# Kernel tuning notes

Hardware: AMD Instinct MI355X
Metric: run time of the kernel (lower is better)

## Reference

```python
import jax, jax.numpy as jnp
import numpy as np

N = 100_000          # nodes
E = 3_200_000        # edges
DIM = 64             # filt_conv_dimension
L = 3                # filt_conv_number
MAX_DEG = 64         # embedding table size = MAX_DEG + 1
SUM_DIMS = DIM * (L + 1)  # 256, fc input
BN_EPS = 1e-5
NEG_SLOPE = 0.01


def _leaky(x):
    return jnp.where(x >= 0, x, NEG_SLOPE * x)


def _batchnorm(x, g, b):
    # training-mode BN over the node axis
    mu = jnp.mean(x, axis=0, keepdims=True)
    var = jnp.var(x, axis=0, keepdims=True)
    return g * (x - mu) * jax.lax.rsqrt(var + BN_EPS) + b


def setup_inputs() -> dict:
    key = jax.random.key(0)
    ks = jax.random.split(key, 16)
    s = 0.05
    inp = {
        "node_deg": jax.random.randint(ks[0], (N,), 0, MAX_DEG, dtype=jnp.int32),
        "edge_index": jax.random.randint(ks[1], (2, E), 0, N, dtype=jnp.int32),
        "embed_deg": jax.random.normal(ks[2], (MAX_DEG + 1, DIM), jnp.float32) * s,
        "eps": jnp.zeros((L,), jnp.float32),
        "W1": jax.random.normal(ks[3], (L, DIM, DIM), jnp.float32) * s,
        "b1": jnp.zeros((L, DIM), jnp.float32),
        "W2": jax.random.normal(ks[4], (L, DIM, DIM), jnp.float32) * s,
        "b2": jnp.zeros((L, DIM), jnp.float32),
        "bn_g": jnp.ones((L, DIM), jnp.float32),
        "bn_b": jnp.zeros((L, DIM), jnp.float32),
        "fc_W1": jax.random.normal(ks[5], (SUM_DIMS, DIM), jnp.float32) * s,
        "fc_b1": jnp.zeros((DIM,), jnp.float32),
        "fc_bn_g": jnp.ones((DIM,), jnp.float32),
        "fc_bn_b": jnp.zeros((DIM,), jnp.float32),
        "fc_W2": jax.random.normal(ks[6], (DIM, 1), jnp.float32) * s,
        "fc_b2": jnp.zeros((1,), jnp.float32),
    }
    return inp


def reference(node_deg, edge_index, embed_deg, eps, W1, b1, W2, b2,
              bn_g, bn_b, fc_W1, fc_b1, fc_bn_g, fc_bn_b, fc_W2, fc_b2):
    src, dst = edge_index[0], edge_index[1]
    h = embed_deg[node_deg]                       # [N, DIM]
    z = [h]
    for l in range(L):
        x = z[-1]
        # GINConv: (1+eps)*x_i + sum_{j->i} x_j, then MLP lin_lrelu_lin
        agg = jax.ops.segment_sum(x[src], dst, num_segments=N)  # [N, DIM]
        m = (1.0 + eps[l]) * x + agg
        h1 = _leaky(m @ W1[l] + b1[l])
        out = h1 @ W2[l] + b2[l]
        out = _leaky(_batchnorm(out, bn_g[l], bn_b[l]))
        z.append(out)
    xcat = jnp.concatenate(z, axis=1)             # [N, SUM_DIMS]
    hfc = _leaky(_batchnorm(xcat @ fc_W1 + fc_b1, fc_bn_g, fc_bn_b))
    ret = jax.nn.sigmoid(hfc @ fc_W2 + fc_b2)     # [N, 1]
    return jnp.squeeze(ret, axis=-1)              # [N]
```

## Files before the change

kernel.cpp:

```cpp
#include <hip/hip_runtime.h>
#include <hip/hip_bf16.h>

#define NN 100000
#define NE 3200000
#define D 64
#define BN_EPS 1e-5f

#define NP 512
#define CHUNK 6250
#define NB 391
#define SPREAD 16

typedef float v2f __attribute__((ext_vector_type(2)));

__global__ __launch_bounds__(256) void embed_kernel(const int* __restrict__ deg,
    const float* __restrict__ emb, float* __restrict__ zcat) {
  int idx = blockIdx.x * 256 + threadIdx.x;
  int i = idx >> 6, d = idx & 63;
  if (i < NN) zcat[(long)i * 256 + d] = emb[(long)deg[i] * D + d];
}

__global__ __launch_bounds__(256) void bucket_kernel(const int* __restrict__ ei,
    int* __restrict__ rec, int* __restrict__ S) {
  __shared__ int cntL[392];
  __shared__ int curL[392];
  __shared__ int scanbuf[256];
  int t = threadIdx.x;
  int p = blockIdx.x;
  int e0 = p * CHUNK;
  cntL[t] = 0;
  if (t < 136) cntL[256 + t] = 0;
  __syncthreads();
  for (int e = t; e < CHUNK; e += 256) {
    int dd = ei[NE + e0 + e];
    atomicAdd(&cntL[(unsigned)dd >> 8], 1);
  }
  __syncthreads();
  int a0 = 0, a1 = 0;
  if (t < 196) { a0 = cntL[2 * t]; a1 = cntL[2 * t + 1]; }
  int s = a0 + a1;
  scanbuf[t] = s;
  __syncthreads();
  for (int off = 1; off < 256; off <<= 1) {
    int x = (t >= off) ? scanbuf[t - off] : 0;
    __syncthreads();
    scanbuf[t] += x;
    __syncthreads();
  }
  int ex = scanbuf[t] - s;
  if (t < 196) {
    curL[2 * t]     = ex;
    curL[2 * t + 1] = ex + a0;
    S[p * 392 + 2 * t]     = e0 + ex;
    S[p * 392 + 2 * t + 1] = e0 + ex + a0;
  }
  __syncthreads();
  for (int e = t; e < CHUNK; e += 256) {
    int ss = ei[e0 + e];
    int dd = ei[NE + e0 + e];
    int b = (unsigned)dd >> 8;
    int pos = atomicAdd(&curL[b], 1);
    rec[e0 + pos] = ss | ((dd & 255) << 17);
  }
}

__global__ __launch_bounds__(256) void bucketsum_kernel(const int* __restrict__ S,
    int* __restrict__ bsum) {
  __shared__ int sh[256];
  int B = blockIdx.x;
  int t = threadIdx.x;
  int c = 0;
  for (int p = t; p < NP; p += 256)
    c += S[p * 392 + B + 1] - S[p * 392 + B];
  sh[t] = c;
  __syncthreads();
  for (int o = 128; o > 0; o >>= 1) {
    if (t < o) sh[t] += sh[t + o];
    __syncthreads();
  }
  if (t == 0) bsum[B] = sh[0];
}

__global__ __launch_bounds__(512) void scan2_kernel(int* __restrict__ bsum) {
  __shared__ int sh[512];
  int t = threadIdx.x;
  int v = (t < NB) ? bsum[t] : 0;
  sh[t] = v;
  __syncthreads();
  for (int o = 1; o < 512; o <<= 1) {
    int x = (t >= o) ? sh[t - o] : 0;
    __syncthreads();
    sh[t] += x;
    __syncthreads();
  }
  if (t < NB) bsum[t] = sh[t] - v;
}

__global__ __launch_bounds__(512) void sort_kernel(const int* __restrict__ rec,
    const int* __restrict__ S, const int* __restrict__ bsum,
    const int* __restrict__ deg,
    int* __restrict__ csroff, int* __restrict__ csrsrc,
    unsigned* __restrict__ cnt8) {
  __shared__ int cntL[256];
  __shared__ int curL[256];
  __shared__ unsigned hist[256 * 65];
  int t = threadIdx.x;
  int B = blockIdx.x;
  if (t < 256) cntL[t] = 0;
  for (int k = t; k < 256 * 65; k += 512) hist[k] = 0;
  __syncthreads();
  int lane = t & 15;
  int g = t >> 4;
  for (int p = g; p < NP; p += 32) {
    int s0 = S[p * 392 + B], s1 = S[p * 392 + B + 1];
    for (int e = s0 + lane; e < s1; e += 16) {
      int r = rec[e];
      int dl = (unsigned)r >> 17;
      atomicAdd(&cntL[dl], 1);
      atomicAdd(&hist[dl * 65 + deg[r & 0x1FFFF]], 1u);
    }
  }
  __syncthreads();
  int v = 0;
  if (t < 256) { v = cntL[t]; curL[t] = v; }
  __syncthreads();
  for (int o = 1; o < 256; o <<= 1) {
    int x = 0;
    if (t < 256 && t >= o) x = curL[t - o];
    __syncthreads();
    if (t < 256) curL[t] += x;
    __syncthreads();
  }
  int b0 = bsum[B];
  if (t < 256) {
    int excl = curL[t] - v;
    int node = B * 256 + t;
    if (node <= NN) csroff[node] = b0 + excl;
  }
  __syncthreads();
  if (t < 256) curL[t] = b0 + (curL[t] - v);
  if (t < 256) {
    int node = B * 256 + t;
    if (node < NN) {
      #pragma unroll
      for (int j = 0; j < 16; j++) {
        unsigned p = (hist[t * 65 + 4 * j] & 255)
                   | ((hist[t * 65 + 4 * j + 1] & 255) << 8)
                   | ((hist[t * 65 + 4 * j + 2] & 255) << 16)
                   | ((hist[t * 65 + 4 * j + 3] & 255) << 24);
        cnt8[(long)node * 16 + j] = p;
      }
    }
  }
  __syncthreads();
  for (int p = g; p < NP; p += 32) {
    int s0 = S[p * 392 + B], s1 = S[p * 392 + B + 1];
    for (int e = s0 + lane; e < s1; e += 16) {
      int r = rec[e];
      int pos = atomicAdd(&curL[(unsigned)r >> 17], 1);
      csrsrc[pos] = r & 0x1FFFF;
    }
  }
}

__global__ __launch_bounds__(256) void agg0_kernel(const unsigned* __restrict__ cnt8,
    const float* __restrict__ emb, float* __restrict__ agg) {
  __shared__ float Es[64][64];
  __shared__ float XsT[64][64];
  int t = threadIdx.x;
  int i0 = blockIdx.x * 64;
  int wr = t >> 4, wc = (t & 15) * 4;
  #pragma unroll
  for (int j = 0; j < 4; j++)
    *(float4*)&Es[wr + 16 * j][wc] = *(const float4*)&emb[(long)(wr + 16 * j) * D + wc];
  {
    int row = t & 63;
    int gi = i0 + row;
    int gis = (gi < NN) ? gi : NN - 1;
    int jb = (t >> 6) * 4;
    #pragma unroll
    for (int j = 0; j < 4; j++) {
      unsigned u = cnt8[(long)gis * 16 + jb + j];
      int k = (jb + j) * 4;
      XsT[k + 0][row] = (float)(u & 255);
      XsT[k + 1][row] = (float)((u >> 8) & 255);
      XsT[k + 2][row] = (float)((u >> 16) & 255);
      XsT[k + 3][row] = (float)(u >> 24);
    }
  }
  int c0 = (t & 15) * 4;
  int r0 = (t >> 4) * 4;
  float4 acc[4];
  #pragma unroll
  for (int r = 0; r < 4; r++) acc[r] = make_float4(0.f, 0.f, 0.f, 0.f);
  __syncthreads();
  #pragma unroll 8
  for (int k = 0; k < 64; k++) {
    float4 w4 = *(const float4*)&Es[k][c0];
    float4 x4 = *(const float4*)&XsT[k][r0];
    acc[0].x += x4.x * w4.x; acc[0].y += x4.x * w4.y; acc[0].z += x4.x * w4.z; acc[0].w += x4.x * w4.w;
    acc[1].x += x4.y * w4.x; acc[1].y += x4.y * w4.y; acc[1].z += x4.y * w4.z; acc[1].w += x4.y * w4.w;
    acc[2].x += x4.z * w4.x; acc[2].y += x4.z * w4.y; acc[2].z += x4.z * w4.z; acc[2].w += x4.z * w4.w;
    acc[3].x += x4.w * w4.x; acc[3].y += x4.w * w4.y; acc[3].z += x4.w * w4.z; acc[3].w += x4.w * w4.w;
  }
  #pragma unroll
  for (int r = 0; r < 4; r++) {
    int gi = i0 + r0 + r;
    if (gi < NN) *(float4*)&agg[(long)gi * D + c0] = acc[r];
  }
}

__global__ __launch_bounds__(256) void agg_kernel(const int* __restrict__ off,
    const int* __restrict__ srcs, const unsigned* __restrict__ xh32,
    float* __restrict__ agg) {
  int t = threadIdx.x;
  int lane = t & 7;
  int g = t >> 3;
  int b = blockIdx.x;
  int slice = b & 1;
  int i = (b >> 1) * 32 + g;
  const unsigned* base = xh32 + (long)slice * NN * 8;
  int e0 = off[i], e1 = off[i + 1];
  float s0 = 0.f, s1 = 0.f, s2 = 0.f, s3 = 0.f;
  int e = e0;
  for (; e + 4 <= e1; e += 4) {
    int j0 = srcs[e + 0], j1 = srcs[e + 1], j2 = srcs[e + 2], j3 = srcs[e + 3];
    unsigned u0 = base[(long)j0 * 8 + lane];
    unsigned u1 = base[(long)j1 * 8 + lane];
    unsigned u2 = base[(long)j2 * 8 + lane];
    unsigned u3 = base[(long)j3 * 8 + lane];
    v2f l0 = __builtin_amdgcn_cvt_pk_f32_fp8((int)u0, false);
    v2f h0 = __builtin_amdgcn_cvt_pk_f32_fp8((int)u0, true);
    v2f l1 = __builtin_amdgcn_cvt_pk_f32_fp8((int)u1, false);
    v2f h1 = __builtin_amdgcn_cvt_pk_f32_fp8((int)u1, true);
    v2f l2 = __builtin_amdgcn_cvt_pk_f32_fp8((int)u2, false);
    v2f h2 = __builtin_amdgcn_cvt_pk_f32_fp8((int)u2, true);
    v2f l3 = __builtin_amdgcn_cvt_pk_f32_fp8((int)u3, false);
    v2f h3 = __builtin_amdgcn_cvt_pk_f32_fp8((int)u3, true);
    s0 += (l0.x + l1.x) + (l2.x + l3.x);
    s1 += (l0.y + l1.y) + (l2.y + l3.y);
    s2 += (h0.x + h1.x) + (h2.x + h3.x);
    s3 += (h0.y + h1.y) + (h2.y + h3.y);
  }
  for (; e < e1; e++) {
    unsigned u = base[(long)srcs[e] * 8 + lane];
    v2f lo = __builtin_amdgcn_cvt_pk_f32_fp8((int)u, false);
    v2f hi = __builtin_amdgcn_cvt_pk_f32_fp8((int)u, true);
    s0 += lo.x; s1 += lo.y; s2 += hi.x; s3 += hi.y;
  }
  *(float4*)&agg[(long)i * D + slice * 32 + lane * 4] = make_float4(s0, s1, s2, s3);
}

__global__ __launch_bounds__(256) void layer_kernel(
    const float* __restrict__ X,
    const float* __restrict__ AGG,
    const float* __restrict__ epsv, int l,
    const float* __restrict__ W1, const float* __restrict__ b1,
    const float* __restrict__ W2, const float* __restrict__ b2,
    float* __restrict__ Z, float* __restrict__ spread)
{
  __shared__ float Ws[64][64];
  __shared__ float XsT[64][64];
  int t = threadIdx.x;
  int i0 = blockIdx.x * 64;
  float alpha = 1.0f + epsv[l];
  int c0 = (t & 15) * 4;
  int r0 = (t >> 4) * 4;
  int wr = t >> 4;
  int wc = (t & 15) * 4;

  #pragma unroll
  for (int j = 0; j < 4; j++)
    *(float4*)&Ws[wr + 16 * j][wc] = *(const float4*)&W1[(long)(wr + 16 * j) * D + wc];
  {
    int row = t & 63;
    int gi = i0 + row;
    int gis = (gi < NN) ? gi : NN - 1;
    int kb = (t >> 6) * 16;
    #pragma unroll
    for (int j = 0; j < 4; j++) {
      int k = kb + 4 * j;
      float4 xv = *(const float4*)&X[(long)gis * 256 + k];
      float4 a4 = *(const float4*)&AGG[(long)gis * D + k];
      xv.x = alpha * xv.x + a4.x;
      xv.y = alpha * xv.y + a4.y;
      xv.z = alpha * xv.z + a4.z;
      xv.w = alpha * xv.w + a4.w;
      XsT[k + 0][row] = xv.x;
      XsT[k + 1][row] = xv.y;
      XsT[k + 2][row] = xv.z;
      XsT[k + 3][row] = xv.w;
    }
  }
  __syncthreads();

  float4 h[4];
  {
    float4 b4 = *(const float4*)&b1[c0];
    #pragma unroll
    for (int r = 0; r < 4; r++) h[r] = b4;
  }
  #pragma unroll 8
  for (int k = 0; k < 64; k++) {
    float4 w4 = *(const float4*)&Ws[k][c0];
    float4 x4 = *(const float4*)&XsT[k][r0];
    h[0].x += x4.x * w4.x; h[0].y += x4.x * w4.y; h[0].z += x4.x * w4.z; h[0].w += x4.x * w4.w;
    h[1].x += x4.y * w4.x; h[1].y += x4.y * w4.y; h[1].z += x4.y * w4.z; h[1].w += x4.y * w4.w;
    h[2].x += x4.z * w4.x; h[2].y += x4.z * w4.y; h[2].z += x4.z * w4.z; h[2].w += x4.z * w4.w;
    h[3].x += x4.w * w4.x; h[3].y += x4.w * w4.y; h[3].z += x4.w * w4.z; h[3].w += x4.w * w4.w;
  }
  #pragma unroll
  for (int r = 0; r < 4; r++) {
    h[r].x = (h[r].x >= 0.0f) ? h[r].x : 0.01f * h[r].x;
    h[r].y = (h[r].y >= 0.0f) ? h[r].y : 0.01f * h[r].y;
    h[r].z = (h[r].z >= 0.0f) ? h[r].z : 0.01f * h[r].z;
    h[r].w = (h[r].w >= 0.0f) ? h[r].w : 0.01f * h[r].w;
  }
  __syncthreads();

  #pragma unroll
  for (int r = 0; r < 4; r++) {
    XsT[c0 + 0][r0 + r] = h[r].x;
    XsT[c0 + 1][r0 + r] = h[r].y;
    XsT[c0 + 2][r0 + r] = h[r].z;
    XsT[c0 + 3][r0 + r] = h[r].w;
  }
  #pragma unroll
  for (int j = 0; j < 4; j++)
    *(float4*)&Ws[wr + 16 * j][wc] = *(const float4*)&W2[(long)(wr + 16 * j) * D + wc];
  __syncthreads();

  float4 z[4];
  {
    float4 b4 = *(const float4*)&b2[c0];
    #pragma unroll
    for (int r = 0; r < 4; r++) z[r] = b4;
  }
  #pragma unroll 8
  for (int k = 0; k < 64; k++) {
    float4 w4 = *(const float4*)&Ws[k][c0];
    float4 x4 = *(const float4*)&XsT[k][r0];
    z[0].x += x4.x * w4.x; z[0].y += x4.x * w4.y; z[0].z += x4.x * w4.z; z[0].w += x4.x * w4.w;
    z[1].x += x4.y * w4.x; z[1].y += x4.y * w4.y; z[1].z += x4.y * w4.z; z[1].w += x4.y * w4.w;
    z[2].x += x4.z * w4.x; z[2].y += x4.z * w4.y; z[2].z += x4.z * w4.z; z[2].w += x4.z * w4.w;
    z[3].x += x4.w * w4.x; z[3].y += x4.w * w4.y; z[3].z += x4.w * w4.z; z[3].w += x4.w * w4.w;
  }
  #pragma unroll
  for (int r = 0; r < 4; r++) {
    int gi = i0 + r0 + r;
    if (gi < NN) *(float4*)&Z[(long)gi * 256 + c0] = z[r];
  }

  float s[4] = {0, 0, 0, 0}, sq[4] = {0, 0, 0, 0};
  #pragma unroll
  for (int r = 0; r < 4; r++) {
    if (i0 + r0 + r < NN) {
      s[0] += z[r].x; sq[0] += z[r].x * z[r].x;
      s[1] += z[r].y; sq[1] += z[r].y * z[r].y;
      s[2] += z[r].z; sq[2] += z[r].z * z[r].z;
      s[3] += z[r].w; sq[3] += z[r].w * z[r].w;
    }
  }
  __syncthreads();
  float* red = &XsT[0][0];
  int grp = t >> 4;
  #pragma unroll
  for (int j = 0; j < 4; j++) {
    red[grp * 64 + c0 + j] = s[j];
    red[1024 + grp * 64 + c0 + j] = sq[j];
  }
  __syncthreads();
  if (t < 64) {
    float a = 0.0f, b = 0.0f;
    #pragma unroll
    for (int g = 0; g < 16; g++) {
      a += red[g * 64 + t];
      b += red[1024 + g * 64 + t];
    }
    int slot = blockIdx.x & (SPREAD - 1);
    atomicAdd(&spread[slot * 128 + t], a);
    atomicAdd(&spread[slot * 128 + 64 + t], b);
  }
}

__global__ __launch_bounds__(256) void fc1_kernel(
    const float* __restrict__ X,
    const float* __restrict__ W, const float* __restrict__ bias,
    float* __restrict__ Y, float* __restrict__ spread)
{
  __shared__ float Ws[64][64];
  __shared__ float XsT[64][64];
  int t = threadIdx.x;
  int i0 = blockIdx.x * 64;
  int c0 = (t & 15) * 4;
  int r0 = (t >> 4) * 4;
  int wr = t >> 4;
  int wc = (t & 15) * 4;

  float4 acc[4];
  {
    float4 b4 = *(const float4*)&bias[c0];
    #pragma unroll
    for (int r = 0; r < 4; r++) acc[r] = b4;
  }
  for (int kc = 0; kc < 256; kc += 64) {
    __syncthreads();
    #pragma unroll
    for (int j = 0; j < 4; j++)
      *(float4*)&Ws[wr + 16 * j][wc] = *(const float4*)&W[(long)(kc + wr + 16 * j) * D + wc];
    {
      int row = t & 63;
      int gi = i0 + row;
      int gis = (gi < NN) ? gi : NN - 1;
      int kb = (t >> 6) * 16;
      #pragma unroll
      for (int j = 0; j < 4; j++) {
        int k = kb + 4 * j;
        float4 xv = *(const float4*)&X[(long)gis * 256 + kc + k];
        XsT[k + 0][row] = xv.x;
        XsT[k + 1][row] = xv.y;
        XsT[k + 2][row] = xv.z;
        XsT[k + 3][row] = xv.w;
      }
    }
    __syncthreads();
    #pragma unroll 8
    for (int k = 0; k < 64; k++) {
      float4 w4 = *(const float4*)&Ws[k][c0];
      float4 x4 = *(const float4*)&XsT[k][r0];
      acc[0].x += x4.x * w4.x; acc[0].y += x4.x * w4.y; acc[0].z += x4.x * w4.z; acc[0].w += x4.x * w4.w;
      acc[1].x += x4.y * w4.x; acc[1].y += x4.y * w4.y; acc[1].z += x4.y * w4.z; acc[1].w += x4.y * w4.w;
      acc[2].x += x4.z * w4.x; acc[2].y += x4.z * w4.y; acc[2].z += x4.z * w4.z; acc[2].w += x4.z * w4.w;
      acc[3].x += x4.w * w4.x; acc[3].y += x4.w * w4.y; acc[3].z += x4.w * w4.z; acc[3].w += x4.w * w4.w;
    }
  }
  #pragma unroll
  for (int r = 0; r < 4; r++) {
    int gi = i0 + r0 + r;
    if (gi < NN) *(float4*)&Y[(long)gi * D + c0] = acc[r];
  }
  float s[4] = {0, 0, 0, 0}, sq[4] = {0, 0, 0, 0};
  #pragma unroll
  for (int r = 0; r < 4; r++) {
    if (i0 + r0 + r < NN) {
      s[0] += acc[r].x; sq[0] += acc[r].x * acc[r].x;
      s[1] += acc[r].y; sq[1] += acc[r].y * acc[r].y;
      s[2] += acc[r].z; sq[2] += acc[r].z * acc[r].z;
      s[3] += acc[r].w; sq[3] += acc[r].w * acc[r].w;
    }
  }
  __syncthreads();
  float* red = &XsT[0][0];
  int grp = t >> 4;
  #pragma unroll
  for (int j = 0; j < 4; j++) {
    red[grp * 64 + c0 + j] = s[j];
    red[1024 + grp * 64 + c0 + j] = sq[j];
  }
  __syncthreads();
  if (t < 64) {
    float a = 0.0f, b = 0.0f;
    #pragma unroll
    for (int g = 0; g < 16; g++) {
      a += red[g * 64 + t];
      b += red[1024 + g * 64 + t];
    }
    int slot = blockIdx.x & (SPREAD - 1);
    atomicAdd(&spread[slot * 128 + t], a);
    atomicAdd(&spread[slot * 128 + 64 + t], b);
  }
}

__global__ __launch_bounds__(128) void bn_finalize_kernel(
    const float* __restrict__ spread, float* __restrict__ statsF) {
  int t = threadIdx.x;
  float a = 0.0f;
  #pragma unroll
  for (int g = 0; g < SPREAD; g++) a += spread[g * 128 + t];
  statsF[t] = a;
}

__global__ __launch_bounds__(256) void bn_apply_kernel(float* __restrict__ Zs,
    const float* __restrict__ stats,
    const float* __restrict__ g, const float* __restrict__ b,
    unsigned short* __restrict__ Outh) {
  int idx = blockIdx.x * 256 + threadIdx.x;
  int i = idx >> 5, dp = (idx & 31) * 2;
  if (i >= NN) return;
  float invn = 1.0f / (float)NN;
  float v0, v1;
  {
    float mu = stats[dp] * invn;
    float var = fmaxf(stats[64 + dp] * invn - mu * mu, 0.0f);
    float sc = g[dp] * rsqrtf(var + BN_EPS);
    v0 = sc * (Zs[(long)i * 256 + dp] - mu) + b[dp];
    v0 = (v0 >= 0.0f) ? v0 : 0.01f * v0;
  }
  {
    float mu = stats[dp + 1] * invn;
    float var = fmaxf(stats[64 + dp + 1] * invn - mu * mu, 0.0f);
    float sc = g[dp + 1] * rsqrtf(var + BN_EPS);
    v1 = sc * (Zs[(long)i * 256 + dp + 1] - mu) + b[dp + 1];
    v1 = (v1 >= 0.0f) ? v1 : 0.01f * v1;
  }
  Zs[(long)i * 256 + dp]     = v0;
  Zs[(long)i * 256 + dp + 1] = v1;
  if (Outh) {
    int packed = __builtin_amdgcn_cvt_pk_fp8_f32(v0, v1, 0, false);
    Outh[(long)(dp >> 5) * NN * 16 + (long)i * 16 + ((dp & 31) >> 1)] =
        (unsigned short)packed;
  }
}

__global__ __launch_bounds__(256) void fc2bn_kernel(const float* __restrict__ H,
    const float* __restrict__ stats,
    const float* __restrict__ g, const float* __restrict__ b,
    const float* __restrict__ W2, const float* __restrict__ b2,
    float* __restrict__ out) {
  int tid = threadIdx.x;
  int k = tid & 63, q = tid >> 6;
  int i = blockIdx.x * 4 + q;
  float invn = 1.0f / (float)NN;
  float mu = stats[k] * invn;
  float var = fmaxf(stats[64 + k] * invn - mu * mu, 0.0f);
  float sc = g[k] * rsqrtf(var + BN_EPS);
  float v = 0.0f;
  if (i < NN) {
    float hv = sc * (H[(long)i * D + k] - mu) + b[k];
    hv = (hv >= 0.0f) ? hv : 0.01f * hv;
    v = hv * W2[k];
  }
  #pragma unroll
  for (int off = 32; off > 0; off >>= 1)
    v += __shfl_down(v, off);
  if (k == 0 && i < NN) {
    float x = v + b2[0];
    out[i] = 1.0f / (1.0f + __expf(-x));
  }
}

extern "C" void kernel_launch(void* const* d_in, const int* in_sizes, int n_in,
                              void* d_out, int out_size, void* d_ws, size_t ws_size,
                              hipStream_t stream) {
  const int*   node_deg   = (const int*)d_in[0];
  const int*   edge_index = (const int*)d_in[1];
  const float* embedw     = (const float*)d_in[2];
  const float* eps        = (const float*)d_in[3];
  const float* W1         = (const float*)d_in[4];
  const float* b1         = (const float*)d_in[5];
  const float* W2         = (const float*)d_in[6];
  const float* b2         = (const float*)d_in[7];
  const float* bn_g       = (const float*)d_in[8];
  const float* bn_b       = (const float*)d_in[9];
  const float* fc_W1      = (const float*)d_in[10];
  const float* fc_b1      = (const float*)d_in[11];
  const float* fc_bn_g    = (const float*)d_in[12];
  const float* fc_bn_b    = (const float*)d_in[13];
  const float* fc_W2      = (const float*)d_in[14];
  const float* fc_b2      = (const float*)d_in[15];

  float* zcat   = (float*)d_ws;
  float* agg    = zcat + (long)NN * 256;
  float* statsS = agg + (long)NN * D;
  float* statsF = statsS + 4 * SPREAD * 128;
  int*   csroff = (int*)(statsF + 512);
  int*   bsum   = csroff + NN + 1;
  int*   csrsrc = bsum + 512;
  int*   rec    = csrsrc + NE;
  int*   S      = rec + NE;
  unsigned* cnt8 = (unsigned*)(S + NP * 392);
  unsigned short* xh = (unsigned short*)rec;

  const int rowBlocks  = NN / 4;
  const int gemmBlocks = (NN + 63) / 64;
  const int aggBlocks  = (NN / 32) * 2;
  const int bnBlocks   = (NN * 32 + 255) / 256;

  bucket_kernel<<<NP, 256, 0, stream>>>(edge_index, rec, S);
  bucketsum_kernel<<<NB, 256, 0, stream>>>(S, bsum);
  scan2_kernel<<<1, 512, 0, stream>>>(bsum);
  sort_kernel<<<NB, 512, 0, stream>>>(rec, S, bsum, node_deg,
      csroff, csrsrc, cnt8);

  hipMemsetAsync(statsS, 0, (size_t)(4 * SPREAD * 128 + 512) * sizeof(float), stream);

  embed_kernel<<<rowBlocks, 256, 0, stream>>>(node_deg, embedw, zcat);

  for (int l = 0; l < 3; ++l) {
    if (l == 0)
      agg0_kernel<<<gemmBlocks, 256, 0, stream>>>(cnt8, embedw, agg);
    else
      agg_kernel<<<aggBlocks, 256, 0, stream>>>(csroff, csrsrc,
          (const unsigned*)xh, agg);
    layer_kernel<<<gemmBlocks, 256, 0, stream>>>(zcat + l * D, agg, eps, l,
        W1 + (long)l * D * D, b1 + (long)l * D,
        W2 + (long)l * D * D, b2 + (long)l * D,
        zcat + (l + 1) * D, statsS + (long)l * SPREAD * 128);
    bn_finalize_kernel<<<1, 128, 0, stream>>>(statsS + (long)l * SPREAD * 128,
        statsF + (long)l * 128);
    bn_apply_kernel<<<bnBlocks, 256, 0, stream>>>(zcat + (l + 1) * D,
        statsF + (long)l * 128, bn_g + (long)l * D, bn_b + (long)l * D,
        (l < 2) ? xh : nullptr);
  }

  fc1_kernel<<<gemmBlocks, 256, 0, stream>>>(zcat, fc_W1, fc_b1, agg,
      statsS + 3L * SPREAD * 128);
  bn_finalize_kernel<<<1, 128, 0, stream>>>(statsS + 3L * SPREAD * 128,
      statsF + 3L * 128);
  fc2bn_kernel<<<rowBlocks, 256, 0, stream>>>(agg, statsF + 3L * 128,
      fc_bn_g, fc_bn_b, fc_W2, fc_b2, (float*)d_out);
}
```

Baseline: 536.7 us.

## Fuse embed and layer-0 aggregation into layer kernel; widen GEMM tiles to 128 rows

Removes the separate embed and agg0 kernels. Layer 0 now computes the count-times-embedding aggregation, writes the embedding slice of zcat, and runs the MLP, all in one kernel. Separately, layer_kernel and fc1_kernel tiles grow from 64 to 128 rows per block, so each thread holds 8 rows of accumulators, which raises register pressure and LDS use. The aim is fewer launches, less global traffic for agg and zcat at layer 0, and more reuse of each weight load, at the cost of lower occupancy and half as many blocks.

```diff
diff --git a/kernel.cpp b/kernel.cpp
--- a/kernel.cpp
+++ b/kernel.cpp
@@ -13,12 +13,9 @@
 
 typedef float v2f __attribute__((ext_vector_type(2)));
 
-__global__ __launch_bounds__(256) void embed_kernel(const int* __restrict__ deg,
-    const float* __restrict__ emb, float* __restrict__ zcat) {
-  int idx = blockIdx.x * 256 + threadIdx.x;
-  int i = idx >> 6, d = idx & 63;
-  if (i < NN) zcat[(long)i * 256 + d] = emb[(long)deg[i] * D + d];
-}
+#define FMA4(accr, xs, w4) \
+  accr.x += (xs) * (w4).x; accr.y += (xs) * (w4).y; \
+  accr.z += (xs) * (w4).z; accr.w += (xs) * (w4).w;
 
 __global__ __launch_bounds__(256) void bucket_kernel(const int* __restrict__ ei,
     int* __restrict__ rec, int* __restrict__ S) {
@@ -160,53 +157,6 @@
       int pos = atomicAdd(&curL[(unsigned)r >> 17], 1);
       csrsrc[pos] = r & 0x1FFFF;
     }
-  }
-}
-
-__global__ __launch_bounds__(256) void agg0_kernel(const unsigned* __restrict__ cnt8,
-    const float* __restrict__ emb, float* __restrict__ agg) {
-  __shared__ float Es[64][64];
-  __shared__ float XsT[64][64];
-  int t = threadIdx.x;
-  int i0 = blockIdx.x * 64;
-  int wr = t >> 4, wc = (t & 15) * 4;
-  #pragma unroll
-  for (int j = 0; j < 4; j++)
-    *(float4*)&Es[wr + 16 * j][wc] = *(const float4*)&emb[(long)(wr + 16 * j) * D + wc];
-  {
-    int row = t & 63;
-    int gi = i0 + row;
-    int gis = (gi < NN) ? gi : NN - 1;
-    int jb = (t >> 6) * 4;
-    #pragma unroll
-    for (int j = 0; j < 4; j++) {
-      unsigned u = cnt8[(long)gis * 16 + jb + j];
-      int k = (jb + j) * 4;
-      XsT[k + 0][row] = (float)(u & 255);
-      XsT[k + 1][row] = (float)((u >> 8) & 255);
-      XsT[k + 2][row] = (float)((u >> 16) & 255);
-      XsT[k + 3][row] = (float)(u >> 24);
-    }
-  }
-  int c0 = (t & 15) * 4;
-  int r0 = (t >> 4) * 4;
-  float4 acc[4];
-  #pragma unroll
-  for (int r = 0; r < 4; r++) acc[r] = make_float4(0.f, 0.f, 0.f, 0.f);
-  __syncthreads();
-  #pragma unroll 8
-  for (int k = 0; k < 64; k++) {
-    float4 w4 = *(const float4*)&Es[k][c0];
-    float4 x4 = *(const float4*)&XsT[k][r0];
-    acc[0].x += x4.x * w4.x; acc[0].y += x4.x * w4.y; acc[0].z += x4.x * w4.z; acc[0].w += x4.x * w4.w;
-    acc[1].x += x4.y * w4.x; acc[1].y += x4.y * w4.y; acc[1].z += x4.y * w4.z; acc[1].w += x4.y * w4.w;
-    acc[2].x += x4.z * w4.x; acc[2].y += x4.z * w4.y; acc[2].z += x4.z * w4.z; acc[2].w += x4.z * w4.w;
-    acc[3].x += x4.w * w4.x; acc[3].y += x4.w * w4.y; acc[3].z += x4.w * w4.z; acc[3].w += x4.w * w4.w;
-  }
-  #pragma unroll
-  for (int r = 0; r < 4; r++) {
-    int gi = i0 + r0 + r;
-    if (gi < NN) *(float4*)&agg[(long)gi * D + c0] = acc[r];
   }
 }
 
@@ -254,72 +204,113 @@
 __global__ __launch_bounds__(256) void layer_kernel(
     const float* __restrict__ X,
     const float* __restrict__ AGG,
+    const unsigned* __restrict__ CNT8, const float* __restrict__ EMB,
+    const int* __restrict__ deg, float* __restrict__ Z0,
     const float* __restrict__ epsv, int l,
     const float* __restrict__ W1, const float* __restrict__ b1,
     const float* __restrict__ W2, const float* __restrict__ b2,
     float* __restrict__ Z, float* __restrict__ spread)
 {
   __shared__ float Ws[64][64];
-  __shared__ float XsT[64][64];
-  int t = threadIdx.x;
-  int i0 = blockIdx.x * 64;
+  __shared__ float XsT[64][128];
+  int t = threadIdx.x;
+  int i0 = blockIdx.x * 128;
   float alpha = 1.0f + epsv[l];
   int c0 = (t & 15) * 4;
-  int r0 = (t >> 4) * 4;
+  int r0 = (t >> 4) * 8;
   int wr = t >> 4;
   int wc = (t & 15) * 4;
-
-  #pragma unroll
-  for (int j = 0; j < 4; j++)
-    *(float4*)&Ws[wr + 16 * j][wc] = *(const float4*)&W1[(long)(wr + 16 * j) * D + wc];
-  {
-    int row = t & 63;
-    int gi = i0 + row;
-    int gis = (gi < NN) ? gi : NN - 1;
-    int kb = (t >> 6) * 16;
-    #pragma unroll
-    for (int j = 0; j < 4; j++) {
+  int row = t & 127;
+  int gi_row = i0 + row;
+  int gis_row = (gi_row < NN) ? gi_row : NN - 1;
+  int kb = (t >> 7) * 32;
+
+  if (CNT8) {
+    #pragma unroll
+    for (int j = 0; j < 4; j++)
+      *(float4*)&Ws[wr + 16 * j][wc] = *(const float4*)&EMB[(long)(wr + 16 * j) * D + wc];
+    #pragma unroll
+    for (int j = 0; j < 8; j++) {
+      unsigned u = CNT8[(long)gis_row * 16 + (kb >> 2) + j];
       int k = kb + 4 * j;
-      float4 xv = *(const float4*)&X[(long)gis * 256 + k];
-      float4 a4 = *(const float4*)&AGG[(long)gis * D + k];
-      xv.x = alpha * xv.x + a4.x;
-      xv.y = alpha * xv.y + a4.y;
-      xv.z = alpha * xv.z + a4.z;
-      xv.w = alpha * xv.w + a4.w;
-      XsT[k + 0][row] = xv.x;
-      XsT[k + 1][row] = xv.y;
-      XsT[k + 2][row] = xv.z;
-      XsT[k + 3][row] = xv.w;
-    }
-  }
-  __syncthreads();
-
-  float4 h[4];
+      XsT[k + 0][row] = (float)(u & 255);
+      XsT[k + 1][row] = (float)((u >> 8) & 255);
+      XsT[k + 2][row] = (float)((u >> 16) & 255);
+      XsT[k + 3][row] = (float)(u >> 24);
+    }
+    __syncthreads();
+    float4 acc[8];
+    #pragma unroll
+    for (int r = 0; r < 8; r++) acc[r] = make_float4(0.f, 0.f, 0.f, 0.f);
+    #pragma unroll 4
+    for (int k = 0; k < 64; k++) {
+      float4 w4 = *(const float4*)&Ws[k][c0];
+      float4 xa = *(const float4*)&XsT[k][r0];
+      float4 xb = *(const float4*)&XsT[k][r0 + 4];
+      FMA4(acc[0], xa.x, w4); FMA4(acc[1], xa.y, w4);
+      FMA4(acc[2], xa.z, w4); FMA4(acc[3], xa.w, w4);
+      FMA4(acc[4], xb.x, w4); FMA4(acc[5], xb.y, w4);
+      FMA4(acc[6], xb.z, w4); FMA4(acc[7], xb.w, w4);
+    }
+    __syncthreads();
+    #pragma unroll
+    for (int r = 0; r < 8; r++) {
+      int gi = i0 + r0 + r;
+      int gis = (gi < NN) ? gi : NN - 1;
+      float4 xv = *(const float4*)&EMB[(long)deg[gis] * D + c0];
+      if (gi < NN) *(float4*)&Z0[(long)gi * 256 + c0] = xv;
+      XsT[c0 + 0][r0 + r] = alpha * xv.x + acc[r].x;
+      XsT[c0 + 1][r0 + r] = alpha * xv.y + acc[r].y;
+      XsT[c0 + 2][r0 + r] = alpha * xv.z + acc[r].z;
+      XsT[c0 + 3][r0 + r] = alpha * xv.w + acc[r].w;
+    }
+    #pragma unroll
+    for (int j = 0; j < 4; j++)
+      *(float4*)&Ws[wr + 16 * j][wc] = *(const float4*)&W1[(long)(wr + 16 * j) * D + wc];
+    __syncthreads();
+  } else {
+    #pragma unroll
+    for (int j = 0; j < 4; j++)
+      *(float4*)&Ws[wr + 16 * j][wc] = *(const float4*)&W1[(long)(wr + 16 * j) * D + wc];
+    #pragma unroll
+    for (int j = 0; j < 8; j++) {
+      int k = kb + 4 * j;
+      float4 xv = *(const float4*)&X[(long)gis_row * 256 + k];
+      float4 a4 = *(const float4*)&AGG[(long)gis_row * D + k];
+      XsT[k + 0][row] = alpha * xv.x + a4.x;
+      XsT[k + 1][row] = alpha * xv.y + a4.y;
+      XsT[k + 2][row] = alpha * xv.z + a4.z;
+      XsT[k + 3][row] = alpha * xv.w + a4.w;
+    }
+    __syncthreads();
+  }
+
+  float4 h[8];
   {
     float4 b4 = *(const float4*)&b1[c0];
     #pragma unroll
-    for (int r = 0; r < 4; r++) h[r] = b4;
-  }
-  #pragma unroll 8
+    for (int r = 0; r < 8; r++) h[r] = b4;
+  }
+  #pragma unroll 4
   for (int k = 0; k < 64; k++) {
     float4 w4 = *(const float4*)&Ws[k][c0];
-    float4 x4 = *(const float4*)&XsT[k][r0];
-    h[0].x += x4.x * w4.x; h[0].y += x4.x * w4.y; h[0].z += x4.x * w4.z; h[0].w += x4.x * w4.w;
-    h[1].x += x4.y * w4.x; h[1].y += x4.y * w4.y; h[1].z += x4.y * w4.z; h[1].w += x4.y * w4.w;
-    h[2].x += x4.z * w4.x; h[2].y += x4.z * w4.y; h[2].z += x4.z * w4.z; h[2].w += x4.z * w4.w;
-    h[3].x += x4.w * w4.x; h[3].y += x4.w * w4.y; h[3].z += x4.w * w4.z; h[3].w += x4.w * w4.w;
-  }
-  #pragma unroll
-  for (int r = 0; r < 4; r++) {
+    float4 xa = *(const float4*)&XsT[k][r0];
+    float4 xb = *(const float4*)&XsT[k][r0 + 4];
+    FMA4(h[0], xa.x, w4); FMA4(h[1], xa.y, w4);
+    FMA4(h[2], xa.z, w4); FMA4(h[3], xa.w, w4);
+    FMA4(h[4], xb.x, w4); FMA4(h[5], xb.y, w4);
+    FMA4(h[6], xb.z, w4); FMA4(h[7], xb.w, w4);
+  }
+  #pragma unroll
+  for (int r = 0; r < 8; r++) {
     h[r].x = (h[r].x >= 0.0f) ? h[r].x : 0.01f * h[r].x;
     h[r].y = (h[r].y >= 0.0f) ? h[r].y : 0.01f * h[r].y;
     h[r].z = (h[r].z >= 0.0f) ? h[r].z : 0.01f * h[r].z;
     h[r].w = (h[r].w >= 0.0f) ? h[r].w : 0.01f * h[r].w;
   }
   __syncthreads();
-
-  #pragma unroll
-  for (int r = 0; r < 4; r++) {
+  #pragma unroll
+  for (int r = 0; r < 8; r++) {
     XsT[c0 + 0][r0 + r] = h[r].x;
     XsT[c0 + 1][r0 + r] = h[r].y;
     XsT[c0 + 2][r0 + r] = h[r].z;
@@ -330,30 +321,31 @@
     *(float4*)&Ws[wr + 16 * j][wc] = *(const float4*)&W2[(long)(wr + 16 * j) * D + wc];
   __syncthreads();
 
-  float4 z[4];
+  float4 z[8];
   {
     float4 b4 = *(const float4*)&b2[c0];
     #pragma unroll
-    for (int r = 0; r < 4; r++) z[r] = b4;
-  }
-  #pragma unroll 8
+    for (int r = 0; r < 8; r++) z[r] = b4;
+  }
+  #pragma unroll 4
   for (int k = 0; k < 64; k++) {
     float4 w4 = *(const float4*)&Ws[k][c0];
-    float4 x4 = *(const float4*)&XsT[k][r0];
-    z[0].x += x4.x * w4.x; z[0].y += x4.x * w4.y; z[0].z += x4.x * w4.z; z[0].w += x4.x * w4.w;
-    z[1].x += x4.y * w4.x; z[1].y += x4.y * w4.y; z[1].z += x4.y * w4.z; z[1].w += x4.y * w4.w;
-    z[2].x += x4.z * w4.x; z[2].y += x4.z * w4.y; z[2].z += x4.z * w4.z; z[2].w += x4.z * w4.w;
-    z[3].x += x4.w * w4.x; z[3].y += x4.w * w4.y; z[3].z += x4.w * w4.z; z[3].w += x4.w * w4.w;
-  }
-  #pragma unroll
-  for (int r = 0; r < 4; r++) {
+    float4 xa = *(const float4*)&XsT[k][r0];
+    float4 xb = *(const float4*)&XsT[k][r0 + 4];
+    FMA4(z[0], xa.x, w4); FMA4(z[1], xa.y, w4);
+    FMA4(z[2], xa.z, w4); FMA4(z[3], xa.w, w4);
+    FMA4(z[4], xb.x, w4); FMA4(z[5], xb.y, w4);
+    FMA4(z[6], xb.z, w4); FMA4(z[7], xb.w, w4);
+  }
+  #pragma unroll
+  for (int r = 0; r < 8; r++) {
     int gi = i0 + r0 + r;
     if (gi < NN) *(float4*)&Z[(long)gi * 256 + c0] = z[r];
   }
 
   float s[4] = {0, 0, 0, 0}, sq[4] = {0, 0, 0, 0};
   #pragma unroll
-  for (int r = 0; r < 4; r++) {
+  for (int r = 0; r < 8; r++) {
     if (i0 + r0 + r < NN) {
       s[0] += z[r].x; sq[0] += z[r].x * z[r].x;
       s[1] += z[r].y; sq[1] += z[r].y * z[r].y;
@@ -389,59 +381,58 @@
     float* __restrict__ Y, float* __restrict__ spread)
 {
   __shared__ float Ws[64][64];
-  __shared__ float XsT[64][64];
-  int t = threadIdx.x;
-  int i0 = blockIdx.x * 64;
+  __shared__ float XsT[64][128];
+  int t = threadIdx.x;
+  int i0 = blockIdx.x * 128;
   int c0 = (t & 15) * 4;
-  int r0 = (t >> 4) * 4;
+  int r0 = (t >> 4) * 8;
   int wr = t >> 4;
   int wc = (t & 15) * 4;
-
-  float4 acc[4];
+  int row = t & 127;
+  int gi_row = i0 + row;
+  int gis_row = (gi_row < NN) ? gi_row : NN - 1;
+  int kb = (t >> 7) * 32;
+
+  float4 acc[8];
   {
     float4 b4 = *(const float4*)&bias[c0];
     #pragma unroll
-    for (int r = 0; r < 4; r++) acc[r] = b4;
+    for (int r = 0; r < 8; r++) acc[r] = b4;
   }
   for (int kc = 0; kc < 256; kc += 64) {
     __syncthreads();
     #pragma unroll
     for (int j = 0; j < 4; j++)
       *(float4*)&Ws[wr + 16 * j][wc] = *(const float4*)&W[(long)(kc + wr + 16 * j) * D + wc];
-    {
-      int row = t & 63;
-      int gi = i0 + row;
-      int gis = (gi < NN) ? gi : NN - 1;
-      int kb = (t >> 6) * 16;
-      #pragma unroll
-      for (int j = 0; j < 4; j++) {
-        int k = kb + 4 * j;
-        float4 xv = *(const float4*)&X[(long)gis * 256 + kc + k];
-        XsT[k + 0][row] = xv.x;
-        XsT[k + 1][row] = xv.y;
-        XsT[k + 2][row] = xv.z;
-        XsT[k + 3][row] = xv.w;
-      }
-    }
-    __syncthreads();
-    #pragma unroll 8
+    #pragma unroll
+    for (int j = 0; j < 8; j++) {
+      int k = kb + 4 * j;
+      float4 xv = *(const float4*)&X[(long)gis_row * 256 + kc + k];
+      XsT[k + 0][row] = xv.x;
+      XsT[k + 1][row] = xv.y;
+      XsT[k + 2][row] = xv.z;
+      XsT[k + 3][row] = xv.w;
+    }
+    __syncthreads();
+    #pragma unroll 4
     for (int k = 0; k < 64; k++) {
       float4 w4 = *(const float4*)&Ws[k][c0];
-      float4 x4 = *(const float4*)&XsT[k][r0];
-      acc[0].x += x4.x * w4.x; acc[0].y += x4.x * w4.y; acc[0].z += x4.x * w4.z; acc[0].w += x4.x * w4.w;
-      acc[1].x += x4.y * w4.x; acc[1].y += x4.y * w4.y; acc[1].z += x4.y * w4.z; acc[1].w += x4.y * w4.w;
-      acc[2].x += x4.z * w4.x; acc[2].y += x4.z * w4.y; acc[2].z += x4.z * w4.z; acc[2].w += x4.z * w4.w;
-      acc[3].x += x4.w * w4.x; acc[3].y += x4.w * w4.y; acc[3].z += x4.w * w4.z; acc[3].w += x4.w * w4.w;
-    }
-  }
-  #pragma unroll
-  for (int r = 0; r < 4; r++) {
+      float4 xa = *(const float4*)&XsT[k][r0];
+      float4 xb = *(const float4*)&XsT[k][r0 + 4];
+      FMA4(acc[0], xa.x, w4); FMA4(acc[1], xa.y, w4);
+      FMA4(acc[2], xa.z, w4); FMA4(acc[3], xa.w, w4);
+      FMA4(acc[4], xb.x, w4); FMA4(acc[5], xb.y, w4);
+      FMA4(acc[6], xb.z, w4); FMA4(acc[7], xb.w, w4);
+    }
+  }
+  #pragma unroll
+  for (int r = 0; r < 8; r++) {
     int gi = i0 + r0 + r;
     if (gi < NN) *(float4*)&Y[(long)gi * D + c0] = acc[r];
   }
   float s[4] = {0, 0, 0, 0}, sq[4] = {0, 0, 0, 0};
   #pragma unroll
-  for (int r = 0; r < 4; r++) {
+  for (int r = 0; r < 8; r++) {
     if (i0 + r0 + r < NN) {
       s[0] += acc[r].x; sq[0] += acc[r].x * acc[r].x;
       s[1] += acc[r].y; sq[1] += acc[r].y * acc[r].y;
@@ -571,10 +562,10 @@
   unsigned* cnt8 = (unsigned*)(S + NP * 392);
   unsigned short* xh = (unsigned short*)rec;
 
-  const int rowBlocks  = NN / 4;
-  const int gemmBlocks = (NN + 63) / 64;
-  const int aggBlocks  = (NN / 32) * 2;
-  const int bnBlocks   = (NN * 32 + 255) / 256;
+  const int rowBlocks   = NN / 4;
+  const int layerBlocks = (NN + 127) / 128;
+  const int aggBlocks   = (NN / 32) * 2;
+  const int bnBlocks    = (NN * 32 + 255) / 256;
 
   bucket_kernel<<<NP, 256, 0, stream>>>(edge_index, rec, S);
   bucketsum_kernel<<<NB, 256, 0, stream>>>(S, bsum);
@@ -584,15 +575,14 @@
 
   hipMemsetAsync(statsS, 0, (size_t)(4 * SPREAD * 128 + 512) * sizeof(float), stream);
 
-  embed_kernel<<<rowBlocks, 256, 0, stream>>>(node_deg, embedw, zcat);
-
   for (int l = 0; l < 3; ++l) {
-    if (l == 0)
-      agg0_kernel<<<gemmBlocks, 256, 0, stream>>>(cnt8, embedw, agg);
-    else
+    if (l > 0)
       agg_kernel<<<aggBlocks, 256, 0, stream>>>(csroff, csrsrc,
           (const unsigned*)xh, agg);
-    layer_kernel<<<gemmBlocks, 256, 0, stream>>>(zcat + l * D, agg, eps, l,
+    layer_kernel<<<layerBlocks, 256, 0, stream>>>(zcat + l * D,
+        (l == 0) ? nullptr : agg,
+        (l == 0) ? cnt8 : nullptr, embedw, node_deg, zcat,
+        eps, l,
         W1 + (long)l * D * D, b1 + (long)l * D,
         W2 + (long)l * D * D, b2 + (long)l * D,
         zcat + (l + 1) * D, statsS + (long)l * SPREAD * 128);
@@ -603,7 +593,7 @@
         (l < 2) ? xh : nullptr);
   }
 
-  fc1_kernel<<<gemmBlocks, 256, 0, stream>>>(zcat, fc_W1, fc_b1, agg,
+  fc1_kernel<<<layerBlocks, 256, 0, stream>>>(zcat, fc_W1, fc_b1, agg,
       statsS + 3L * SPREAD * 128);
   bn_finalize_kernel<<<1, 128, 0, stream>>>(statsS + 3L * SPREAD * 128,
       statsF + 3L * 128);
```

After: 537.0 us. Within noise of the previous version (+0.1%).
